# Kernel optimization log

Measured on AMD Instinct MI355X. Metric: run time of the kernel, lower is better.

## Reference

```python
import jax, jax.numpy as jnp
import numpy as np
from jax import lax

K = 3
STRIDE = 1
PAD = 1
DIL = 1


def setup_inputs() -> dict:
    key = jax.random.key(0)
    k1, k2, k3 = jax.random.split(key, 3)
    B, C, H, W = 8, 128, 64, 64
    O = 128
    x = jax.random.normal(k1, (B, C, H, W), jnp.float32)
    # offset-predicting conv weights (small init -> small offsets, as in DCN practice)
    w_off = jax.random.normal(k2, (2 * K * K, C, K, K), jnp.float32) * 0.01
    b_off = jnp.zeros((2 * K * K,), jnp.float32)
    # deformable conv weight [O, Cin, K, K], bias=False in the source
    w = jax.random.normal(k3, (O, C, K, K), jnp.float32) * (1.0 / np.sqrt(C * K * K))
    return {"x": x, "w_off": w_off, "b_off": b_off, "w": w}


def _deform_conv(x, offset, w):
    # x: [B,C,H,W]; offset: [B, 2*K*K, Ho, Wo]; w: [O,C,K,K]
    B, C, H, W = x.shape
    Ho, Wo = offset.shape[2], offset.shape[3]
    K2 = K * K
    off = offset.reshape(B, K2, 2, Ho, Wo)
    oy, ox = off[:, :, 0], off[:, :, 1]            # [B,K2,Ho,Wo]
    ky = (jnp.arange(K2) // K).astype(jnp.float32)  # kernel row per tap
    kx = (jnp.arange(K2) % K).astype(jnp.float32)
    base_y = (jnp.arange(Ho) * STRIDE - PAD).astype(jnp.float32)
    base_x = (jnp.arange(Wo) * STRIDE - PAD).astype(jnp.float32)
    py = base_y[None, None, :, None] + ky[None, :, None, None] * DIL + oy
    px = base_x[None, None, None, :] + kx[None, :, None, None] * DIL + ox

    y0 = jnp.floor(py)
    x0 = jnp.floor(px)
    dy = py - y0
    dx = px - x0
    y0i = y0.astype(jnp.int32)
    x0i = x0.astype(jnp.int32)
    bidx = jnp.arange(B)[:, None, None, None]

    def gather(yi, xi):
        valid = (yi >= 0) & (yi < H) & (xi >= 0) & (xi < W)
        yc = jnp.clip(yi, 0, H - 1)
        xc = jnp.clip(xi, 0, W - 1)
        v = x[bidx, :, yc, xc]  # [B,K2,Ho,Wo,C]
        return v * valid[..., None]

    v00 = gather(y0i, x0i)
    v01 = gather(y0i, x0i + 1)
    v10 = gather(y0i + 1, x0i)
    v11 = gather(y0i + 1, x0i + 1)
    samp = (v00 * ((1 - dy) * (1 - dx))[..., None]
            + v01 * ((1 - dy) * dx)[..., None]
            + v10 * (dy * (1 - dx))[..., None]
            + v11 * (dy * dx)[..., None])  # [B,K2,Ho,Wo,C]

    O = w.shape[0]
    return jnp.einsum('bkhwc,ock->bohw', samp, w.reshape(O, C, K2))


def reference(x, w_off, b_off, w):
    # offset conv: standard conv2d, stride/pad/dilation as in __init__
    offset = lax.conv_general_dilated(
        x, w_off, window_strides=(STRIDE, STRIDE),
        padding=[(PAD, PAD), (PAD, PAD)], rhs_dilation=(DIL, DIL))
    offset = offset + b_off[None, :, None, None]
    return _deform_conv(x, offset, w)
```

## Files before the change

kernel.cpp:

```cpp
#include <hip/hip_runtime.h>

#define B_ 8
#define C_ 128
#define H_ 64
#define W_ 64
#define O_ 128
#define F_ 18
#define K2_ 9
#define HW_ 4096
#define CK2_ 1152

#define WR_ 10
#define WC_ 22

typedef __attribute__((ext_vector_type(8))) short short8_t;
typedef __attribute__((ext_vector_type(4))) float f32x4_t;
typedef __attribute__((ext_vector_type(2))) float f32x2_t;
typedef __attribute__((ext_vector_type(4))) unsigned int uint4_t;

__device__ inline short bf16r(float f) {
  unsigned u = __builtin_bit_cast(unsigned, f);
  u += 0x7FFFu + ((u >> 16) & 1u);
  return (short)(u >> 16);
}
__device__ inline f32x2_t pk_mul(f32x2_t a, f32x2_t b) {
  f32x2_t d;
  asm("v_pk_mul_f32 %0, %1, %2" : "=v"(d) : "v"(a), "v"(b));
  return d;
}
__device__ inline f32x2_t pk_fma(f32x2_t a, f32x2_t b, f32x2_t c) {
  f32x2_t d;
  asm("v_pk_fma_f32 %0, %1, %2, %3" : "=v"(d) : "v"(a), "v"(b), "v"(c));
  return d;
}
__device__ inline f32x2_t bfpair(unsigned u) {
  return (f32x2_t){__builtin_bit_cast(float, u << 16),
                   __builtin_bit_cast(float, u)};
}

__global__ __launch_bounds__(256) void prep_all_kernel(
    const float* __restrict__ w, const float* __restrict__ w_off,
    const float* __restrict__ x,
    short* __restrict__ w_bt2, short* __restrict__ w_ot2,
    short* __restrict__ x_t) {
  __shared__ float tile[128][65];
  int bid = blockIdx.x, t = threadIdx.x;
  if (bid < 576) {
    int i = bid * 256 + t;
    int kk2 = i & 31, o = (i >> 5) & 127, ks = i >> 12;
    w_bt2[i] = bf16r(w[(o * C_ + (ks & 3) * 32 + kk2) * K2_ + (ks >> 2)]);
  } else if (bid < 720) {
    int i = (bid - 576) * 256 + t;
    int kk2 = i & 31, f = (i >> 5) & 31, ks = i >> 10;
    w_ot2[i] = (f < F_) ? bf16r(w_off[(f * C_ + (ks & 3) * 32 + kk2) * K2_ + (ks >> 2)])
                        : (short)0;
  } else {
    int xb_id = bid - 720;
    int b = xb_id >> 6;
    int p_base = (xb_id & 63) << 6;
    const float* xb = x + ((long)b << 19);
#pragma unroll
    for (int i = 0; i < 32; ++i) {
      int idx = (i << 8) + t;
      int c = idx >> 6, p = idx & 63;
      tile[c][p] = xb[((long)c << 12) + p_base + p];
    }
    __syncthreads();
#pragma unroll
    for (int i = 0; i < 32; ++i) {
      int idx = (i << 8) + t;
      int p = idx >> 7, c = idx & 127;
      x_t[(((long)(b << 12) + p_base + p) << 7) + c] = bf16r(tile[c][p]);
    }
  }
}

__device__ inline short8_t lds16(const short* xs, int pix, int ch) {
  return *(const short8_t*)(xs + (pix << 7) + ((ch ^ (pix & 15)) << 3));
}

__global__ __launch_bounds__(512, 4) void fused_deform_kernel(
    const short* __restrict__ x_t, const short* __restrict__ w_ot2,
    const float* __restrict__ b_off, const short* __restrict__ w_bt2,
    float* __restrict__ out) {
  __shared__ short xs[WR_ * WC_ * 128];
  __shared__ float offs[4][16][20];

  int tid = threadIdx.x;
  int wv = tid >> 6, lane = tid & 63;
  int row = wv & 3, g = wv >> 2;
  int fr = lane & 15, q = lane >> 4;
  int bid = (int)blockIdx.x;
  int b = bid & 7;
  int tile_id = bid >> 3;
  int ho0 = (tile_id >> 2) << 2;
  int x0b = (tile_id & 3) << 4;
  int ys  = min(max(ho0 - 3, 0), H_ - WR_);
  int xsL = min(max(x0b - 3, 0), W_ - WC_);
  int ye2 = ys + WR_ - 1, xe2 = xsL + WC_ - 1;

  const short* xtb = x_t + ((long)b << 19);

#pragma unroll
  for (int i = 0; i < 7; ++i) {
    int ci = (i << 9) + tid;
    if (ci < WR_ * WC_ * 16) {
      int pix = ci >> 4, ch = ci & 15;
      int yr = pix / WC_, xr = pix - yr * WC_;
      short8_t v = *(const short8_t*)(xtb + ((((ys + yr) << 6) + xsL + xr) << 7) + (ch << 3));
      *(short8_t*)(xs + (pix << 7) + ((ch ^ (pix & 15)) << 3)) = v;
    }
  }
  __syncthreads();

  int ho = ho0 + row;
  int wo = x0b + fr;

  {
    f32x4_t oacc0 = (f32x4_t){0.f, 0.f, 0.f, 0.f};
    f32x4_t oacc1 = (f32x4_t){0.f, 0.f, 0.f, 0.f};
#pragma unroll
    for (int kt = 0; kt < 9; ++kt) {
      int y = ho + kt / 3 - 1, xx = wo + kt % 3 - 1;
      bool ok = (y >= 0) & (y < H_) & (xx >= 0) & (xx < W_);
      int yc = min(max(y, 0), H_ - 1), xc = min(max(xx, 0), W_ - 1);
      int pixA = (yc - ys) * WC_ + (xc - xsL);
#pragma unroll
      for (int sh = 0; sh < 2; ++sh) {
        int s = (g << 1) | sh;
        short8_t bfv = lds16(xs, pixA, (s << 2) + q);
        if (!ok) bfv = (short8_t){0, 0, 0, 0, 0, 0, 0, 0};
        int ks = (kt << 2) + s;
        short8_t a0 = *(const short8_t*)(w_ot2 + (((ks << 5) + fr) << 5) + (q << 3));
        short8_t a1 = *(const short8_t*)(w_ot2 + (((ks << 5) + 16 + fr) << 5) + (q << 3));
        oacc0 = __builtin_amdgcn_mfma_f32_16x16x32_bf16(a0, bfv, oacc0, 0, 0, 0);
        oacc1 = __builtin_amdgcn_mfma_f32_16x16x32_bf16(a1, bfv, oacc1, 0, 0, 0);
      }
    }
    if (g == 0) {
#pragma unroll
      for (int r = 0; r < 4; ++r) {
        int f0 = (q << 2) + r;
        offs[row][fr][f0] = oacc0[r] + b_off[f0];
      }
      if (q == 0) {
        offs[row][fr][16] = oacc1[0] + b_off[16];
        offs[row][fr][17] = oacc1[1] + b_off[17];
      }
    }
    __syncthreads();
    if (g == 1) {
#pragma unroll
      for (int r = 0; r < 4; ++r) {
        int f0 = (q << 2) + r;
        offs[row][fr][f0] += oacc0[r];
      }
      if (q == 0) {
        offs[row][fr][16] += oacc1[0];
        offs[row][fr][17] += oacc1[1];
      }
    }
  }
  __syncthreads();

  f32x4_t acc[8];
#pragma unroll
  for (int nf = 0; nf < 8; ++nf) acc[nf] = (f32x4_t){0.f, 0.f, 0.f, 0.f};

#pragma unroll
  for (int kt = 0; kt < 9; ++kt) {
    float oy = offs[row][fr][2 * kt];
    float ox = offs[row][fr][2 * kt + 1];

    float py = (float)(ho + kt / 3 - 1) + oy;
    float px = (float)(wo + kt % 3 - 1) + ox;
    float fy0 = floorf(py), fx0 = floorf(px);
    float dy = py - fy0, dx = px - fx0;
    int y0 = (int)fy0, x0 = (int)fx0;
    int y1 = y0 + 1, x1 = x0 + 1;
    float my0 = (y0 >= 0 && y0 < H_) ? 1.f : 0.f;
    float my1 = (y1 >= 0 && y1 < H_) ? 1.f : 0.f;
    float mx0 = (x0 >= 0 && x0 < W_) ? 1.f : 0.f;
    float mx1 = (x1 >= 0 && x1 < W_) ? 1.f : 0.f;
    float w00 = (1.f - dy) * (1.f - dx) * my0 * mx0;
    float w01 = (1.f - dy) * dx * my0 * mx1;
    float w10 = dy * (1.f - dx) * my1 * mx0;
    float w11 = dy * dx * my1 * mx1;
    int y0c = min(max(y0, 0), H_ - 1), y1c = min(max(y1, 0), H_ - 1);
    int x0c = min(max(x0, 0), W_ - 1), x1c = min(max(x1, 0), W_ - 1);
    int p00 = (y0c - ys) * WC_ + (x0c - xsL), p01 = p00 + (x1c - x0c);
    int p10 = (y1c - ys) * WC_ + (x0c - xsL), p11 = p10 + (x1c - x0c);

    f32x2_t w00p = (f32x2_t){w00, w00}, w01p = (f32x2_t){w01, w01};
    f32x2_t w10p = (f32x2_t){w10, w10}, w11p = (f32x2_t){w11, w11};

    short8_t v00[2], v01[2], v10[2], v11[2];
    unsigned long long bad =
        __ballot((y0c < ys) || (y1c > ye2) || (x0c < xsL) || (x1c > xe2));
    if (bad == 0ULL) {
#pragma unroll
      for (int sh = 0; sh < 2; ++sh) {
        int s = (g << 1) | sh;
        int ch = (s << 2) + q;
        v00[sh] = lds16(xs, p00, ch);
        v01[sh] = lds16(xs, p01, ch);
        v10[sh] = lds16(xs, p10, ch);
        v11[sh] = lds16(xs, p11, ch);
      }
    } else {
      const short* g00 = xtb + (((y0c << 6) + x0c) << 7);
      const short* g01 = xtb + (((y0c << 6) + x1c) << 7);
      const short* g10 = xtb + (((y1c << 6) + x0c) << 7);
      const short* g11 = xtb + (((y1c << 6) + x1c) << 7);
#pragma unroll
      for (int sh = 0; sh < 2; ++sh) {
        int s = (g << 1) | sh;
        int c0 = (s << 5) + (q << 3);
        v00[sh] = *(const short8_t*)(g00 + c0);
        v01[sh] = *(const short8_t*)(g01 + c0);
        v10[sh] = *(const short8_t*)(g10 + c0);
        v11[sh] = *(const short8_t*)(g11 + c0);
      }
    }

#pragma unroll
    for (int sh = 0; sh < 2; ++sh) {
      int s = (g << 1) | sh;
      uint4_t u00 = __builtin_bit_cast(uint4_t, v00[sh]);
      uint4_t u01 = __builtin_bit_cast(uint4_t, v01[sh]);
      uint4_t u10 = __builtin_bit_cast(uint4_t, v10[sh]);
      uint4_t u11 = __builtin_bit_cast(uint4_t, v11[sh]);
      uint4_t sfu;
#pragma unroll
      for (int d = 0; d < 4; ++d) {
        f32x2_t r = pk_mul(bfpair(u00[d]), w00p);
        r = pk_fma(bfpair(u01[d]), w01p, r);
        r = pk_fma(bfpair(u10[d]), w10p, r);
        r = pk_fma(bfpair(u11[d]), w11p, r);
        unsigned p;
        asm("v_cvt_pk_bf16_f32 %0, %1, %2" : "=v"(p) : "v"(r[0]), "v"(r[1]));
        sfu[d] = p;
      }
      short8_t sf = __builtin_bit_cast(short8_t, sfu);
      int ks = (kt << 2) + s;
      const short* wp = w_bt2 + (((ks << 7) + fr) << 5) + (q << 3);
#pragma unroll
      for (int nf = 0; nf < 8; ++nf) {
        short8_t wf = *(const short8_t*)(wp + (nf << 9));
        acc[nf] = __builtin_amdgcn_mfma_f32_16x16x32_bf16(wf, sf, acc[nf], 0, 0, 0);
      }
    }
  }

  __syncthreads();
  float* red = (float*)xs;
  if (g == 1) {
#pragma unroll
    for (int nf = 0; nf < 8; ++nf) {
      *(f32x4_t*)&red[(row * 16 + fr) * 136 + (nf << 4) + (q << 2)] = acc[nf];
    }
  }
  __syncthreads();
  if (g == 0) {
    float* ob = out + ((long)(b * O_) << 12) + (ho << 6) + wo;
#pragma unroll
    for (int nf = 0; nf < 8; ++nf) {
      f32x4_t other = *(const f32x4_t*)&red[(row * 16 + fr) * 136 + (nf << 4) + (q << 2)];
#pragma unroll
      for (int r = 0; r < 4; ++r) {
        ob[(long)((nf << 4) + (q << 2) + r) << 12] = acc[nf][r] + other[r];
      }
    }
  }
}

extern "C" void kernel_launch(void* const* d_in, const int* in_sizes, int n_in,
                              void* d_out, int out_size, void* d_ws, size_t ws_size,
                              hipStream_t stream) {
  const float* x     = (const float*)d_in[0];
  const float* w_off = (const float*)d_in[1];
  const float* b_off = (const float*)d_in[2];
  const float* w     = (const float*)d_in[3];
  float* out = (float*)d_out;

  short* w_bt2 = (short*)d_ws;
  short* w_ot2 = (short*)((char*)d_ws + 294912);
  short* x_t   = (short*)((char*)d_ws + 294912 + 73728);

  prep_all_kernel<<<1232, 256, 0, stream>>>(w, w_off, x, w_bt2, w_ot2, x_t);
  fused_deform_kernel<<<512, 512, 0, stream>>>(x_t, w_ot2, b_off, w_bt2, out);
}
```

Before: 59.77 us.

## Remap waves to two rows by half output channels to reuse weight fragments

Reassigns the deformable-conv phase so each wave samples two output rows and multiplies by only half of the output channels. Each loaded weight fragment now feeds two MFMAs, halving weight fetches. In exchange, bilinear sampling and interpolation is duplicated across the two channel halves, raising VALU and LDS gather work. The cross-group reduction layout is reorganized to match.

```diff
diff --git a/kernel.cpp b/kernel.cpp
--- a/kernel.cpp
+++ b/kernel.cpp
@@ -88,7 +88,6 @@
 
   int tid = threadIdx.x;
   int wv = tid >> 6, lane = tid & 63;
-  int row = wv & 3, g = wv >> 2;
   int fr = lane & 15, q = lane >> 4;
   int bid = (int)blockIdx.x;
   int b = bid & 7;
@@ -113,21 +112,21 @@
   }
   __syncthreads();
 
-  int ho = ho0 + row;
-  int wo = x0b + fr;
-
   {
+    int rowA = wv & 3, gA = wv >> 2;
+    int hoA = ho0 + rowA;
+    int woA = x0b + fr;
     f32x4_t oacc0 = (f32x4_t){0.f, 0.f, 0.f, 0.f};
     f32x4_t oacc1 = (f32x4_t){0.f, 0.f, 0.f, 0.f};
 #pragma unroll
     for (int kt = 0; kt < 9; ++kt) {
-      int y = ho + kt / 3 - 1, xx = wo + kt % 3 - 1;
+      int y = hoA + kt / 3 - 1, xx = woA + kt % 3 - 1;
       bool ok = (y >= 0) & (y < H_) & (xx >= 0) & (xx < W_);
       int yc = min(max(y, 0), H_ - 1), xc = min(max(xx, 0), W_ - 1);
       int pixA = (yc - ys) * WC_ + (xc - xsL);
 #pragma unroll
       for (int sh = 0; sh < 2; ++sh) {
-        int s = (g << 1) | sh;
+        int s = (gA << 1) | sh;
         short8_t bfv = lds16(xs, pixA, (s << 2) + q);
         if (!ok) bfv = (short8_t){0, 0, 0, 0, 0, 0, 0, 0};
         int ks = (kt << 2) + s;
@@ -137,138 +136,161 @@
         oacc1 = __builtin_amdgcn_mfma_f32_16x16x32_bf16(a1, bfv, oacc1, 0, 0, 0);
       }
     }
-    if (g == 0) {
+    if (gA == 0) {
 #pragma unroll
       for (int r = 0; r < 4; ++r) {
         int f0 = (q << 2) + r;
-        offs[row][fr][f0] = oacc0[r] + b_off[f0];
+        offs[rowA][fr][f0] = oacc0[r] + b_off[f0];
       }
       if (q == 0) {
-        offs[row][fr][16] = oacc1[0] + b_off[16];
-        offs[row][fr][17] = oacc1[1] + b_off[17];
+        offs[rowA][fr][16] = oacc1[0] + b_off[16];
+        offs[rowA][fr][17] = oacc1[1] + b_off[17];
       }
     }
     __syncthreads();
-    if (g == 1) {
+    if (gA == 1) {
 #pragma unroll
       for (int r = 0; r < 4; ++r) {
         int f0 = (q << 2) + r;
-        offs[row][fr][f0] += oacc0[r];
+        offs[rowA][fr][f0] += oacc0[r];
       }
       if (q == 0) {
-        offs[row][fr][16] += oacc1[0];
-        offs[row][fr][17] += oacc1[1];
+        offs[rowA][fr][16] += oacc1[0];
+        offs[rowA][fr][17] += oacc1[1];
       }
     }
   }
   __syncthreads();
 
+  int rp = wv & 1, g = (wv >> 1) & 1, h = wv >> 2;
+  int wo = x0b + fr;
+
   f32x4_t acc[8];
 #pragma unroll
-  for (int nf = 0; nf < 8; ++nf) acc[nf] = (f32x4_t){0.f, 0.f, 0.f, 0.f};
+  for (int i = 0; i < 8; ++i) acc[i] = (f32x4_t){0.f, 0.f, 0.f, 0.f};
 
 #pragma unroll
   for (int kt = 0; kt < 9; ++kt) {
-    float oy = offs[row][fr][2 * kt];
-    float ox = offs[row][fr][2 * kt + 1];
-
-    float py = (float)(ho + kt / 3 - 1) + oy;
-    float px = (float)(wo + kt % 3 - 1) + ox;
-    float fy0 = floorf(py), fx0 = floorf(px);
-    float dy = py - fy0, dx = px - fx0;
-    int y0 = (int)fy0, x0 = (int)fx0;
-    int y1 = y0 + 1, x1 = x0 + 1;
-    float my0 = (y0 >= 0 && y0 < H_) ? 1.f : 0.f;
-    float my1 = (y1 >= 0 && y1 < H_) ? 1.f : 0.f;
-    float mx0 = (x0 >= 0 && x0 < W_) ? 1.f : 0.f;
-    float mx1 = (x1 >= 0 && x1 < W_) ? 1.f : 0.f;
-    float w00 = (1.f - dy) * (1.f - dx) * my0 * mx0;
-    float w01 = (1.f - dy) * dx * my0 * mx1;
-    float w10 = dy * (1.f - dx) * my1 * mx0;
-    float w11 = dy * dx * my1 * mx1;
-    int y0c = min(max(y0, 0), H_ - 1), y1c = min(max(y1, 0), H_ - 1);
-    int x0c = min(max(x0, 0), W_ - 1), x1c = min(max(x1, 0), W_ - 1);
-    int p00 = (y0c - ys) * WC_ + (x0c - xsL), p01 = p00 + (x1c - x0c);
-    int p10 = (y1c - ys) * WC_ + (x0c - xsL), p11 = p10 + (x1c - x0c);
-
-    f32x2_t w00p = (f32x2_t){w00, w00}, w01p = (f32x2_t){w01, w01};
-    f32x2_t w10p = (f32x2_t){w10, w10}, w11p = (f32x2_t){w11, w11};
-
-    short8_t v00[2], v01[2], v10[2], v11[2];
-    unsigned long long bad =
-        __ballot((y0c < ys) || (y1c > ye2) || (x0c < xsL) || (x1c > xe2));
-    if (bad == 0ULL) {
+    short8_t sf[2][2];
+#pragma unroll
+    for (int grp = 0; grp < 2; ++grp) {
+      int rowg = (rp << 1) | grp;
+      int ho = ho0 + rowg;
+      float oy = offs[rowg][fr][2 * kt];
+      float ox = offs[rowg][fr][2 * kt + 1];
+      float py = (float)(ho + kt / 3 - 1) + oy;
+      float px = (float)(wo + kt % 3 - 1) + ox;
+      float fy0 = floorf(py), fx0 = floorf(px);
+      float dy = py - fy0, dx = px - fx0;
+      int y0 = (int)fy0, x0 = (int)fx0;
+      int y1 = y0 + 1, x1 = x0 + 1;
+      float my0 = (y0 >= 0 && y0 < H_) ? 1.f : 0.f;
+      float my1 = (y1 >= 0 && y1 < H_) ? 1.f : 0.f;
+      float mx0 = (x0 >= 0 && x0 < W_) ? 1.f : 0.f;
+      float mx1 = (x1 >= 0 && x1 < W_) ? 1.f : 0.f;
+      float w00 = (1.f - dy) * (1.f - dx) * my0 * mx0;
+      float w01 = (1.f - dy) * dx * my0 * mx1;
+      float w10 = dy * (1.f - dx) * my1 * mx0;
+      float w11 = dy * dx * my1 * mx1;
+      int y0c = min(max(y0, 0), H_ - 1), y1c = min(max(y1, 0), H_ - 1);
+      int x0c = min(max(x0, 0), W_ - 1), x1c = min(max(x1, 0), W_ - 1);
+      int p00 = (y0c - ys) * WC_ + (x0c - xsL), p01 = p00 + (x1c - x0c);
+      int p10 = (y1c - ys) * WC_ + (x0c - xsL), p11 = p10 + (x1c - x0c);
+
+      f32x2_t w00p = (f32x2_t){w00, w00}, w01p = (f32x2_t){w01, w01};
+      f32x2_t w10p = (f32x2_t){w10, w10}, w11p = (f32x2_t){w11, w11};
+
+      short8_t v00[2], v01[2], v10[2], v11[2];
+      unsigned long long bad =
+          __ballot((y0c < ys) || (y1c > ye2) || (x0c < xsL) || (x1c > xe2));
+      if (bad == 0ULL) {
+#pragma unroll
+        for (int sh = 0; sh < 2; ++sh) {
+          int ch = (((g << 1) | sh) << 2) + q;
+          v00[sh] = lds16(xs, p00, ch);
+          v01[sh] = lds16(xs, p01, ch);
+          v10[sh] = lds16(xs, p10, ch);
+          v11[sh] = lds16(xs, p11, ch);
+        }
+      } else {
+        const short* g00 = xtb + (((y0c << 6) + x0c) << 7);
+        const short* g01 = xtb + (((y0c << 6) + x1c) << 7);
+        const short* g10 = xtb + (((y1c << 6) + x0c) << 7);
+        const short* g11 = xtb + (((y1c << 6) + x1c) << 7);
+#pragma unroll
+        for (int sh = 0; sh < 2; ++sh) {
+          int c0 = (((g << 1) | sh) << 5) + (q << 3);
+          v00[sh] = *(const short8_t*)(g00 + c0);
+          v01[sh] = *(const short8_t*)(g01 + c0);
+          v10[sh] = *(const short8_t*)(g10 + c0);
+          v11[sh] = *(const short8_t*)(g11 + c0);
+        }
+      }
+
 #pragma unroll
       for (int sh = 0; sh < 2; ++sh) {
-        int s = (g << 1) | sh;
-        int ch = (s << 2) + q;
-        v00[sh] = lds16(xs, p00, ch);
-        v01[sh] = lds16(xs, p01, ch);
-        v10[sh] = lds16(xs, p10, ch);
-        v11[sh] = lds16(xs, p11, ch);
-      }
-    } else {
-      const short* g00 = xtb + (((y0c << 6) + x0c) << 7);
-      const short* g01 = xtb + (((y0c << 6) + x1c) << 7);
-      const short* g10 = xtb + (((y1c << 6) + x0c) << 7);
-      const short* g11 = xtb + (((y1c << 6) + x1c) << 7);
-#pragma unroll
-      for (int sh = 0; sh < 2; ++sh) {
-        int s = (g << 1) | sh;
-        int c0 = (s << 5) + (q << 3);
-        v00[sh] = *(const short8_t*)(g00 + c0);
-        v01[sh] = *(const short8_t*)(g01 + c0);
-        v10[sh] = *(const short8_t*)(g10 + c0);
-        v11[sh] = *(const short8_t*)(g11 + c0);
+        uint4_t u00 = __builtin_bit_cast(uint4_t, v00[sh]);
+        uint4_t u01 = __builtin_bit_cast(uint4_t, v01[sh]);
+        uint4_t u10 = __builtin_bit_cast(uint4_t, v10[sh]);
+        uint4_t u11 = __builtin_bit_cast(uint4_t, v11[sh]);
+        uint4_t sfu;
+#pragma unroll
+        for (int d = 0; d < 4; ++d) {
+          f32x2_t r = pk_mul(bfpair(u00[d]), w00p);
+          r = pk_fma(bfpair(u01[d]), w01p, r);
+          r = pk_fma(bfpair(u10[d]), w10p, r);
+          r = pk_fma(bfpair(u11[d]), w11p, r);
+          unsigned p;
+          asm("v_cvt_pk_bf16_f32 %0, %1, %2" : "=v"(p) : "v"(r[0]), "v"(r[1]));
+          sfu[d] = p;
+        }
+        sf[grp][sh] = __builtin_bit_cast(short8_t, sfu);
       }
     }
 
 #pragma unroll
     for (int sh = 0; sh < 2; ++sh) {
       int s = (g << 1) | sh;
-      uint4_t u00 = __builtin_bit_cast(uint4_t, v00[sh]);
-      uint4_t u01 = __builtin_bit_cast(uint4_t, v01[sh]);
-      uint4_t u10 = __builtin_bit_cast(uint4_t, v10[sh]);
-      uint4_t u11 = __builtin_bit_cast(uint4_t, v11[sh]);
-      uint4_t sfu;
-#pragma unroll
-      for (int d = 0; d < 4; ++d) {
-        f32x2_t r = pk_mul(bfpair(u00[d]), w00p);
-        r = pk_fma(bfpair(u01[d]), w01p, r);
-        r = pk_fma(bfpair(u10[d]), w10p, r);
-        r = pk_fma(bfpair(u11[d]), w11p, r);
-        unsigned p;
-        asm("v_cvt_pk_bf16_f32 %0, %1, %2" : "=v"(p) : "v"(r[0]), "v"(r[1]));
-        sfu[d] = p;
-      }
-      short8_t sf = __builtin_bit_cast(short8_t, sfu);
       int ks = (kt << 2) + s;
-      const short* wp = w_bt2 + (((ks << 7) + fr) << 5) + (q << 3);
-#pragma unroll
-      for (int nf = 0; nf < 8; ++nf) {
+      const short* wp = w_bt2 + (((ks << 7) + (h << 6) + fr) << 5) + (q << 3);
+#pragma unroll
+      for (int nf = 0; nf < 4; ++nf) {
         short8_t wf = *(const short8_t*)(wp + (nf << 9));
-        acc[nf] = __builtin_amdgcn_mfma_f32_16x16x32_bf16(wf, sf, acc[nf], 0, 0, 0);
+        acc[0 * 4 + nf] = __builtin_amdgcn_mfma_f32_16x16x32_bf16(wf, sf[0][sh], acc[0 * 4 + nf], 0, 0, 0);
+        acc[1 * 4 + nf] = __builtin_amdgcn_mfma_f32_16x16x32_bf16(wf, sf[1][sh], acc[1 * 4 + nf], 0, 0, 0);
       }
     }
   }
 
   __syncthreads();
   float* red = (float*)xs;
+  int zone = (rp << 1) + h;
+  int base = zone * 2176;
   if (g == 1) {
 #pragma unroll
-    for (int nf = 0; nf < 8; ++nf) {
-      *(f32x4_t*)&red[(row * 16 + fr) * 136 + (nf << 4) + (q << 2)] = acc[nf];
+    for (int grp = 0; grp < 2; ++grp) {
+#pragma unroll
+      for (int nf = 0; nf < 4; ++nf) {
+        *(f32x4_t*)&red[base + grp * 1088 + fr * 68 + (nf << 4) + (q << 2)] =
+            acc[grp * 4 + nf];
+      }
     }
   }
   __syncthreads();
   if (g == 0) {
-    float* ob = out + ((long)(b * O_) << 12) + (ho << 6) + wo;
-#pragma unroll
-    for (int nf = 0; nf < 8; ++nf) {
-      f32x4_t other = *(const f32x4_t*)&red[(row * 16 + fr) * 136 + (nf << 4) + (q << 2)];
-#pragma unroll
-      for (int r = 0; r < 4; ++r) {
-        ob[(long)((nf << 4) + (q << 2) + r) << 12] = acc[nf][r] + other[r];
+#pragma unroll
+    for (int grp = 0; grp < 2; ++grp) {
+      int rowg = (rp << 1) | grp;
+      int ho = ho0 + rowg;
+      float* ob = out + ((long)(b * O_) << 12) + (ho << 6) + wo;
+#pragma unroll
+      for (int nf = 0; nf < 4; ++nf) {
+        f32x4_t other = *(const f32x4_t*)&red[base + grp * 1088 + fr * 68 + (nf << 4) + (q << 2)];
+#pragma unroll
+        for (int r = 0; r < 4; ++r) {
+          ob[(long)(((h << 6) + (nf << 4) + (q << 2) + r)) << 12] =
+              acc[grp * 4 + nf][r] + other[r];
+        }
       }
     }
   }
```

Result: faster. 55.60 us (-7.0%).
